# Performance work log

Hardware: AMD Instinct MI355X
Metric: run time of the kernel (lower is better)

The kernel has to match this reference:

```python
import jax, jax.numpy as jnp
import numpy as np

N, E, D, L = 100000, 1_600_000, 128, 8


def setup_inputs() -> dict:
    key = jax.random.key(0)
    k0, k1, k2 = jax.random.split(key, 3)
    x = jax.random.normal(k0, (N, D), dtype=jnp.float32)
    edge_index = jax.random.randint(k1, (2, E), 0, N, dtype=jnp.int64)
    Ws = jax.random.normal(k2, (L, D, D), dtype=jnp.float32) / np.float32(np.sqrt(D))
    bs = jnp.zeros((L, D), dtype=jnp.float32)
    return {"x": x, "edge_index": edge_index, "Ws": Ws, "bs": bs}


def _gcn_conv(h, W, b, src, dst, norm_edge, self_norm):
    """PyG GCNConv: linear -> sym-normalized aggregate (with self loops) -> +bias."""
    h = h @ W                                    # [N, D]
    msg = h[src] * norm_edge[:, None]            # [E, D] gather + scale
    agg = jax.ops.segment_sum(msg, dst, num_segments=h.shape[0])  # scatter-add
    return agg + h * self_norm[:, None] + b      # self-loop term fused in


def reference(x, edge_index, Ws, bs):
    src, dst = edge_index[0], edge_index[1]
    # degree of (A + I) on target nodes, symmetric normalization
    deg = jax.ops.segment_sum(jnp.ones((src.shape[0],), jnp.float32), dst,
                              num_segments=x.shape[0]) + 1.0
    dis = deg ** -0.5                            # deg >= 1, safe
    norm_edge = dis[src] * dis[dst]              # per-edge norm
    self_norm = dis * dis                        # per-node self-loop norm

    n_layers = Ws.shape[0]
    h = x
    initial = x
    for i in range(n_layers):
        h = _gcn_conv(h, Ws[i], bs[i], src, dst, norm_edge, self_norm)
        if i > 0:
            h = h + initial
            initial = h
        h = jax.nn.relu(h)
        if i < n_layers - 1:
            # NOTE: at i == 0 the original indexes layers[-1] (last layer) — faithful.
            j = i - 1
            h = h + _gcn_conv(h, Ws[j], bs[j], src, dst, norm_edge, self_norm)
    return h
```

## Files before the change

### kernel.cpp

```cpp
#include <hip/hip_runtime.h>

#define D 128
#define SCAN_CH 1024
#define SA_STRIDE 136
#define SC_STRIDE 132
#define NPB 64
#define CONV_THREADS 512

typedef _Float16 f16x8 __attribute__((ext_vector_type(8)));
typedef float f32x4 __attribute__((ext_vector_type(4)));


__global__ void hist_kernel(const int* __restrict__ dst, int* __restrict__ counts,
                            int E, int N) {
  int range = blockIdx.x & 7;
  int lo = (int)(((long long)N * range) >> 3);
  int hi = (int)(((long long)N * (range + 1)) >> 3);
  int stride = (gridDim.x >> 3) * blockDim.x;
  for (int e = (blockIdx.x >> 3) * blockDim.x + threadIdx.x; e < E; e += stride) {
    int d = dst[e];
    if (d >= lo && d < hi) atomicAdd(&counts[d], 1);
  }
}

__global__ void fill_kernel(const int* __restrict__ src, const int* __restrict__ dst,
    int* __restrict__ fillp, int* __restrict__ csr_src, int E, int N) {
  int range = blockIdx.x & 7;
  int lo = (int)(((long long)N * range) >> 3);
  int hi = (int)(((long long)N * (range + 1)) >> 3);
  int stride = (gridDim.x >> 3) * blockDim.x;
  for (int e = (blockIdx.x >> 3) * blockDim.x + threadIdx.x; e < E; e += stride) {
    int d = dst[e];
    if (d >= lo && d < hi) {
      int s = src[e];
      int p = atomicAdd(&fillp[d], 1);
      csr_src[p] = s;
    }
  }
}

__global__ void dis_kernel(const int* __restrict__ counts, float* __restrict__ dis, int N) {
  int n = blockIdx.x * blockDim.x + threadIdx.x;
  if (n < N) dis[n] = rsqrtf((float)counts[n] + 1.0f);
}

__global__ __launch_bounds__(256) void scan_phaseA(const int* __restrict__ counts,
    int* __restrict__ blksum, int N) {
  __shared__ int red[256];
  int base = blockIdx.x * SCAN_CH;
  int t = threadIdx.x;
  int s = 0;
  #pragma unroll
  for (int j = 0; j < 4; ++j) {
    int idx = base + t * 4 + j;
    if (idx < N) s += counts[idx];
  }
  red[t] = s;
  __syncthreads();
  for (int d = 128; d > 0; d >>= 1) {
    if (t < d) red[t] += red[t + d];
    __syncthreads();
  }
  if (t == 0) blksum[blockIdx.x] = red[0];
}

__global__ __launch_bounds__(1024) void scan_phaseB(int* __restrict__ blksum, int NB) {
  __shared__ int sa[1024], sb[1024];
  int t = threadIdx.x;
  int v = (t < NB) ? blksum[t] : 0;
  sa[t] = v;
  __syncthreads();
  int* a = sa; int* b = sb;
  for (int d = 1; d < 1024; d <<= 1) {
    int val = a[t] + ((t >= d) ? a[t - d] : 0);
    b[t] = val;
    __syncthreads();
    int* tmp = a; a = b; b = tmp;
  }
  if (t < NB) blksum[t] = a[t] - v;
}

__global__ __launch_bounds__(256) void scan_phaseC(const int* __restrict__ counts,
    const int* __restrict__ blksum, int* __restrict__ row_ptr, int* __restrict__ fillp, int N) {
  __shared__ int ra[256], rb[256];
  int base = blockIdx.x * SCAN_CH;
  int t = threadIdx.x;
  int v[4]; int s = 0;
  #pragma unroll
  for (int j = 0; j < 4; ++j) {
    int idx = base + t * 4 + j;
    v[j] = (idx < N) ? counts[idx] : 0;
    s += v[j];
  }
  ra[t] = s;
  __syncthreads();
  int* a = ra; int* b = rb;
  for (int d = 1; d < 256; d <<= 1) {
    int val = a[t] + ((t >= d) ? a[t - d] : 0);
    b[t] = val;
    __syncthreads();
    int* tmp = a; a = b; b = tmp;
  }
  int excl = a[t] - s + blksum[blockIdx.x];
  #pragma unroll
  for (int j = 0; j < 4; ++j) {
    int idx = base + t * 4 + j;
    if (idx < N) {
      row_ptr[idx] = excl;
      fillp[idx] = excl;
      excl += v[j];
      if (idx == N - 1) row_ptr[N] = excl;
    }
  }
}


__global__ void conv_x_kernel(const float* __restrict__ x, const float* __restrict__ dis,
    _Float16* __restrict__ hs, int total8) {
  int i = blockIdx.x * blockDim.x + threadIdx.x;
  if (i >= total8) return;
  int node = i >> 4;
  float dn = dis[node];
  const float4* p = (const float4*)(x + (size_t)i * 8);
  float4 a = p[0], b = p[1];
  f16x8 v;
  v[0] = (_Float16)(dn * a.x); v[1] = (_Float16)(dn * a.y);
  v[2] = (_Float16)(dn * a.z); v[3] = (_Float16)(dn * a.w);
  v[4] = (_Float16)(dn * b.x); v[5] = (_Float16)(dn * b.y);
  v[6] = (_Float16)(dn * b.z); v[7] = (_Float16)(dn * b.w);
  *(f16x8*)(hs + (size_t)i * 8) = v;
}

__global__ void repack_w_kernel(const float* __restrict__ Ws, _Float16* __restrict__ Wf, int total) {
  int t = blockIdx.x * blockDim.x + threadIdx.x;
  if (t >= total) return;
  int lane = t & 63;
  int nb = (t >> 6) & 7;
  int kb = (t >> 9) & 3;
  int l = t >> 11;
  int col = nb * 16 + (lane & 15);
  int k0 = kb * 32 + (lane >> 4) * 8;
  const float* w = Ws + (size_t)l * D * D;
  f16x8 v;
  #pragma unroll
  for (int j = 0; j < 8; ++j) v[j] = (_Float16)w[(k0 + j) * D + col];
  *(f16x8*)(Wf + (size_t)t * 8) = v;
}

__global__ __launch_bounds__(CONV_THREADS) void conv_fused_kernel(
    const _Float16* __restrict__ hs, const int* __restrict__ row_ptr,
    const int* __restrict__ csr_src, const float* __restrict__ dis,
    const f16x8* __restrict__ Wf, const float* __restrict__ bias,
    const float* __restrict__ init_in, float* __restrict__ init_out,
    float* __restrict__ out, _Float16* __restrict__ hs_out, int N, int flags) {
  __shared__ __align__(16) char smem[NPB * SC_STRIDE * 4];
  _Float16* sA = (_Float16*)smem;
  float* sC = (float*)smem;
  int tid = threadIdx.x;
  int node0 = blockIdx.x * NPB;
  int ng = tid >> 4;
  int li = tid & 15;
  int c0 = li * 8;

  #pragma unroll
  for (int k = 0; k < 2; ++k) {
    int lr = ng + 32 * k;
    int n = node0 + lr;
    f16x8 g = {};
    if (n < N) {
      float acc[8];
      #pragma unroll
      for (int j = 0; j < 8; ++j) acc[j] = 0.f;
      int beg = row_ptr[n], end = row_ptr[n + 1];
      #pragma unroll 4
      for (int e = beg; e < end; ++e) {
        int s = csr_src[e];
        f16x8 v = *(const f16x8*)&hs[(size_t)s * D + c0];
        #pragma unroll
        for (int j = 0; j < 8; ++j) acc[j] += (float)v[j];
      }
      f16x8 own = *(const f16x8*)&hs[(size_t)n * D + c0];
      float dn = dis[n];
      #pragma unroll
      for (int j = 0; j < 8; ++j) g[j] = (_Float16)(dn * (acc[j] + (float)own[j]));
    }
    *(f16x8*)&sA[lr * SA_STRIDE + c0] = g;
  }

  int wave = tid >> 6, lane = tid & 63;
  f16x8 bf[4];
  #pragma unroll
  for (int kb = 0; kb < 4; ++kb)
    bf[kb] = Wf[(kb * 8 + wave) * 64 + lane];
  __syncthreads();

  f32x4 ca[4];
  #pragma unroll
  for (int rt = 0; rt < 4; ++rt) ca[rt] = (f32x4){0, 0, 0, 0};
  #pragma unroll
  for (int rt = 0; rt < 4; ++rt) {
    #pragma unroll
    for (int kb = 0; kb < 4; ++kb) {
      f16x8 a = *(const f16x8*)&sA[(rt * 16 + (lane & 15)) * SA_STRIDE + kb * 32 + (lane >> 4) * 8];
      ca[rt] = __builtin_amdgcn_mfma_f32_16x16x32_f16(a, bf[kb], ca[rt], 0, 0, 0);
    }
  }
  __syncthreads();

  {
    int colb = wave * 16 + (lane & 15);
    int rowb = (lane >> 4) * 4;
    #pragma unroll
    for (int rt = 0; rt < 4; ++rt)
      #pragma unroll
      for (int r = 0; r < 4; ++r)
        sC[(rt * 16 + rowb + r) * SC_STRIDE + colb] = ca[rt][r];
  }
  __syncthreads();

  float4 b0 = *(const float4*)&bias[c0];
  float4 b1 = *(const float4*)&bias[c0 + 4];
  #pragma unroll
  for (int k = 0; k < 2; ++k) {
    int lr = ng + 32 * k;
    int n = node0 + lr;
    if (n >= N) continue;
    float v[8];
    float4 s0 = *(const float4*)&sC[lr * SC_STRIDE + c0];
    float4 s1 = *(const float4*)&sC[lr * SC_STRIDE + c0 + 4];
    v[0] = s0.x + b0.x; v[1] = s0.y + b0.y; v[2] = s0.z + b0.z; v[3] = s0.w + b0.w;
    v[4] = s1.x + b1.x; v[5] = s1.y + b1.y; v[6] = s1.z + b1.z; v[7] = s1.w + b1.w;
    size_t off = (size_t)n * D + c0;
    if (flags & 1) {
      float4 i0 = *(const float4*)&init_in[off];
      float4 i1 = *(const float4*)&init_in[off + 4];
      v[0] += i0.x; v[1] += i0.y; v[2] += i0.z; v[3] += i0.w;
      v[4] += i1.x; v[5] += i1.y; v[6] += i1.z; v[7] += i1.w;
    }
    if (flags & 2) {
      *(float4*)&init_out[off]     = make_float4(v[0], v[1], v[2], v[3]);
      *(float4*)&init_out[off + 4] = make_float4(v[4], v[5], v[6], v[7]);
    }
    if (flags & 4) {
      #pragma unroll
      for (int j = 0; j < 8; ++j) v[j] = fmaxf(v[j], 0.f);
    }
    if (flags & 8) {
      float4 p0 = *(const float4*)&out[off];
      float4 p1 = *(const float4*)&out[off + 4];
      v[0] += p0.x; v[1] += p0.y; v[2] += p0.z; v[3] += p0.w;
      v[4] += p1.x; v[5] += p1.y; v[6] += p1.z; v[7] += p1.w;
    }
    *(float4*)&out[off]     = make_float4(v[0], v[1], v[2], v[3]);
    *(float4*)&out[off + 4] = make_float4(v[4], v[5], v[6], v[7]);
    if (flags & 16) {
      float dn = dis[n];
      f16x8 h8;
      #pragma unroll
      for (int j = 0; j < 8; ++j) h8[j] = (_Float16)(dn * v[j]);
      *(f16x8*)&hs_out[off] = h8;
    }
  }
}


extern "C" void kernel_launch(void* const* d_in, const int* in_sizes, int n_in,
                              void* d_out, int out_size, void* d_ws, size_t ws_size,
                              hipStream_t stream) {
  const float* x = (const float*)d_in[0];
  const int* ei = (const int*)d_in[1];
  const float* Ws = (const float*)d_in[2];
  const float* bs = (const float*)d_in[3];
  float* out = (float*)d_out;

  const int N = in_sizes[0] / D;
  const int E = in_sizes[1] / 2;
  const int L = in_sizes[2] / (D * D);
  const int* src = ei;
  const int* dst = ei + E;

  uintptr_t p = (uintptr_t)d_ws;
  auto alloc = [&](size_t bytes) {
    uintptr_t r = p;
    p = (r + bytes + 255) & ~(uintptr_t)255;
    return r;
  };
  float*     dis      = (float*)alloc((size_t)N * 4);
  int*       counts   = (int*)  alloc((size_t)N * 4);
  int*       row_ptr  = (int*)  alloc((size_t)(N + 1) * 4);
  int*       fillp    = (int*)  alloc((size_t)N * 4);
  int*       blksum   = (int*)  alloc((size_t)1024 * 4);
  int*       csr_src  = (int*)  alloc((size_t)E * 4);
  _Float16*  hs_a     = (_Float16*)alloc((size_t)N * D * 2);
  _Float16*  hs_b     = (_Float16*)alloc((size_t)N * D * 2);
  float*     init_buf = (float*)alloc((size_t)N * D * 4);
  _Float16*  Wf       = (_Float16*)alloc((size_t)L * 4 * 8 * 64 * 8 * 2);

  const int NB = (N + SCAN_CH - 1) / SCAN_CH;

  hipMemsetAsync(counts, 0, (size_t)N * 4, stream);
  hist_kernel<<<8 * 192, 256, 0, stream>>>(dst, counts, E, N);
  dis_kernel<<<(N + 255) / 256, 256, 0, stream>>>(counts, dis, N);
  scan_phaseA<<<NB, 256, 0, stream>>>(counts, blksum, N);
  scan_phaseB<<<1, 1024, 0, stream>>>(blksum, NB);
  scan_phaseC<<<NB, 256, 0, stream>>>(counts, blksum, row_ptr, fillp, N);
  fill_kernel<<<8 * 192, 256, 0, stream>>>(src, dst, fillp, csr_src, E, N);
  conv_x_kernel<<<(N * 16 + 255) / 256, 256, 0, stream>>>(x, dis, hs_a, N * 16);
  {
    int total = L * 2048;
    repack_w_kernel<<<(total + 255) / 256, 256, 0, stream>>>(Ws, Wf, total);
  }

  const int conv_grid = (N + NPB - 1) / NPB;
  _Float16* hsp[2] = {hs_a, hs_b};
  int cur = 0;

  for (int i = 0; i < L; ++i) {
    int flags;
    if (i == 0)          flags = 4 | 16;
    else if (i == L - 1) flags = 1 | 4;
    else                 flags = 1 | 2 | 4 | 16;
    const float* init_in = (i <= 1) ? x : (const float*)init_buf;
    conv_fused_kernel<<<conv_grid, CONV_THREADS, 0, stream>>>(hsp[cur], row_ptr, csr_src, dis,
        (const f16x8*)(Wf + (size_t)i * 2048 * 8), bs + (size_t)i * D,
        init_in, init_buf, out, hsp[cur ^ 1], N, flags);
    if (flags & 16) cur ^= 1;
    if (i < L - 1) {
      int j = (i == 0) ? (L - 1) : (i - 1);
      conv_fused_kernel<<<conv_grid, CONV_THREADS, 0, stream>>>(hsp[cur], row_ptr, csr_src, dis,
          (const f16x8*)(Wf + (size_t)j * 2048 * 8), bs + (size_t)j * D,
          nullptr, nullptr, out, hsp[cur ^ 1], N, 8 | 16);
      cur ^= 1;
    }
  }
}
```

Before: 1.323 ms.

## Recover residual from fp16 scaled features instead of fp32 output round-trip

The residual term h that the second conv adds back is now rebuilt from the fp16 scaled features it already loads (own * sqrt(deg)), instead of re-reading the fp32 output buffer. A per-node sqrt(deg) is stored next to dis as a float2. The fp32 output is written only in the final layer, so intermediate kernels skip fp32 reads and writes of the N x D tensor. The residual now carries fp16 rounding and depends on reconstructing h from hs, which adds small numerical error.

```diff
diff --git a/kernel.cpp b/kernel.cpp
--- a/kernel.cpp
+++ b/kernel.cpp
@@ -39,9 +39,12 @@
   }
 }
 
-__global__ void dis_kernel(const int* __restrict__ counts, float* __restrict__ dis, int N) {
+__global__ void dis_kernel(const int* __restrict__ counts, float2* __restrict__ dnr, int N) {
   int n = blockIdx.x * blockDim.x + threadIdx.x;
-  if (n < N) dis[n] = rsqrtf((float)counts[n] + 1.0f);
+  if (n < N) {
+    float c = (float)counts[n] + 1.0f;
+    dnr[n] = make_float2(rsqrtf(c), sqrtf(c));
+  }
 }
 
 __global__ __launch_bounds__(256) void scan_phaseA(const int* __restrict__ counts,
@@ -115,12 +118,12 @@
 }
 
 
-__global__ void conv_x_kernel(const float* __restrict__ x, const float* __restrict__ dis,
+__global__ void conv_x_kernel(const float* __restrict__ x, const float2* __restrict__ dnr,
     _Float16* __restrict__ hs, int total8) {
   int i = blockIdx.x * blockDim.x + threadIdx.x;
   if (i >= total8) return;
   int node = i >> 4;
-  float dn = dis[node];
+  float dn = dnr[node].x;
   const float4* p = (const float4*)(x + (size_t)i * 8);
   float4 a = p[0], b = p[1];
   f16x8 v;
@@ -149,7 +152,7 @@
 
 __global__ __launch_bounds__(CONV_THREADS) void conv_fused_kernel(
     const _Float16* __restrict__ hs, const int* __restrict__ row_ptr,
-    const int* __restrict__ csr_src, const float* __restrict__ dis,
+    const int* __restrict__ csr_src, const float2* __restrict__ dnr,
     const f16x8* __restrict__ Wf, const float* __restrict__ bias,
     const float* __restrict__ init_in, float* __restrict__ init_out,
     float* __restrict__ out, _Float16* __restrict__ hs_out, int N, int flags) {
@@ -162,6 +165,9 @@
   int li = tid & 15;
   int c0 = li * 8;
 
+  float2 dr[2];
+  f16x8 ownr[2];
+
   #pragma unroll
   for (int k = 0; k < 2; ++k) {
     int lr = ng + 32 * k;
@@ -180,9 +186,11 @@
         for (int j = 0; j < 8; ++j) acc[j] += (float)v[j];
       }
       f16x8 own = *(const f16x8*)&hs[(size_t)n * D + c0];
-      float dn = dis[n];
-      #pragma unroll
-      for (int j = 0; j < 8; ++j) g[j] = (_Float16)(dn * (acc[j] + (float)own[j]));
+      float2 d2 = dnr[n];
+      dr[k] = d2;
+      ownr[k] = own;
+      #pragma unroll
+      for (int j = 0; j < 8; ++j) g[j] = (_Float16)(d2.x * (acc[j] + (float)own[j]));
     }
     *(f16x8*)&sA[lr * SA_STRIDE + c0] = g;
   }
@@ -231,6 +239,11 @@
     v[0] = s0.x + b0.x; v[1] = s0.y + b0.y; v[2] = s0.z + b0.z; v[3] = s0.w + b0.w;
     v[4] = s1.x + b1.x; v[5] = s1.y + b1.y; v[6] = s1.z + b1.z; v[7] = s1.w + b1.w;
     size_t off = (size_t)n * D + c0;
+    if (flags & 8) {
+      float rd = dr[k].y;
+      #pragma unroll
+      for (int j = 0; j < 8; ++j) v[j] += (float)ownr[k][j] * rd;
+    }
     if (flags & 1) {
       float4 i0 = *(const float4*)&init_in[off];
       float4 i1 = *(const float4*)&init_in[off + 4];
@@ -245,16 +258,12 @@
       #pragma unroll
       for (int j = 0; j < 8; ++j) v[j] = fmaxf(v[j], 0.f);
     }
-    if (flags & 8) {
-      float4 p0 = *(const float4*)&out[off];
-      float4 p1 = *(const float4*)&out[off + 4];
-      v[0] += p0.x; v[1] += p0.y; v[2] += p0.z; v[3] += p0.w;
-      v[4] += p1.x; v[5] += p1.y; v[6] += p1.z; v[7] += p1.w;
-    }
-    *(float4*)&out[off]     = make_float4(v[0], v[1], v[2], v[3]);
-    *(float4*)&out[off + 4] = make_float4(v[4], v[5], v[6], v[7]);
+    if (flags & 32) {
+      *(float4*)&out[off]     = make_float4(v[0], v[1], v[2], v[3]);
+      *(float4*)&out[off + 4] = make_float4(v[4], v[5], v[6], v[7]);
+    }
     if (flags & 16) {
-      float dn = dis[n];
+      float dn = dr[k].x;
       f16x8 h8;
       #pragma unroll
       for (int j = 0; j < 8; ++j) h8[j] = (_Float16)(dn * v[j]);
@@ -285,7 +294,7 @@
     p = (r + bytes + 255) & ~(uintptr_t)255;
     return r;
   };
-  float*     dis      = (float*)alloc((size_t)N * 4);
+  float2*    dnr      = (float2*)alloc((size_t)N * 8);
   int*       counts   = (int*)  alloc((size_t)N * 4);
   int*       row_ptr  = (int*)  alloc((size_t)(N + 1) * 4);
   int*       fillp    = (int*)  alloc((size_t)N * 4);
@@ -300,12 +309,12 @@
 
   hipMemsetAsync(counts, 0, (size_t)N * 4, stream);
   hist_kernel<<<8 * 192, 256, 0, stream>>>(dst, counts, E, N);
-  dis_kernel<<<(N + 255) / 256, 256, 0, stream>>>(counts, dis, N);
+  dis_kernel<<<(N + 255) / 256, 256, 0, stream>>>(counts, dnr, N);
   scan_phaseA<<<NB, 256, 0, stream>>>(counts, blksum, N);
   scan_phaseB<<<1, 1024, 0, stream>>>(blksum, NB);
   scan_phaseC<<<NB, 256, 0, stream>>>(counts, blksum, row_ptr, fillp, N);
   fill_kernel<<<8 * 192, 256, 0, stream>>>(src, dst, fillp, csr_src, E, N);
-  conv_x_kernel<<<(N * 16 + 255) / 256, 256, 0, stream>>>(x, dis, hs_a, N * 16);
+  conv_x_kernel<<<(N * 16 + 255) / 256, 256, 0, stream>>>(x, dnr, hs_a, N * 16);
   {
     int total = L * 2048;
     repack_w_kernel<<<(total + 255) / 256, 256, 0, stream>>>(Ws, Wf, total);
@@ -318,16 +327,16 @@
   for (int i = 0; i < L; ++i) {
     int flags;
     if (i == 0)          flags = 4 | 16;
-    else if (i == L - 1) flags = 1 | 4;
+    else if (i == L - 1) flags = 1 | 4 | 32;
     else                 flags = 1 | 2 | 4 | 16;
     const float* init_in = (i <= 1) ? x : (const float*)init_buf;
-    conv_fused_kernel<<<conv_grid, CONV_THREADS, 0, stream>>>(hsp[cur], row_ptr, csr_src, dis,
+    conv_fused_kernel<<<conv_grid, CONV_THREADS, 0, stream>>>(hsp[cur], row_ptr, csr_src, dnr,
         (const f16x8*)(Wf + (size_t)i * 2048 * 8), bs + (size_t)i * D,
         init_in, init_buf, out, hsp[cur ^ 1], N, flags);
     if (flags & 16) cur ^= 1;
     if (i < L - 1) {
       int j = (i == 0) ? (L - 1) : (i - 1);
-      conv_fused_kernel<<<conv_grid, CONV_THREADS, 0, stream>>>(hsp[cur], row_ptr, csr_src, dis,
+      conv_fused_kernel<<<conv_grid, CONV_THREADS, 0, stream>>>(hsp[cur], row_ptr, csr_src, dnr,
           (const f16x8*)(Wf + (size_t)j * 2048 * 8), bs + (size_t)j * D,
           nullptr, nullptr, out, hsp[cur ^ 1], N, 8 | 16);
       cur ^= 1;
```

Measured after the change: 1.290 ms. 2.5% less time.
